# Kernel tuning notes

Hardware: AMD Instinct MI355X
Metric: run time of the kernel (lower is better)

The kernel has to match this reference:

```python
import jax, jax.numpy as jnp
import numpy as np

HEADS = 16

def setup_inputs() -> dict:
    key = jax.random.key(0)
    ks = jax.random.split(key, 8)
    S, B, D = 2048, 2, 1024
    scale = 0.02
    return {
        'query': jax.random.normal(ks[0], (S, B, D), jnp.float32),
        'key':   jax.random.normal(ks[1], (S, B, D), jnp.float32),
        'value': jax.random.normal(ks[2], (S, B, D), jnp.float32),
        'Wq': jax.random.normal(ks[3], (D, D), jnp.float32) * scale,
        'bq': jnp.zeros((D,), jnp.float32),
        'Wk': jax.random.normal(ks[4], (D, D), jnp.float32) * scale,
        'bk': jnp.zeros((D,), jnp.float32),
        'Wv': jax.random.normal(ks[5], (D, D), jnp.float32) * scale,
        'bv': jnp.zeros((D,), jnp.float32),
        'Wo': jax.random.normal(ks[6], (D, D), jnp.float32) * scale,
        'bo': jnp.zeros((D,), jnp.float32),
    }

def reference(query, key, value, Wq, bq, Wk, bk, Wv, bv, Wo, bo):
    S, B, D = query.shape
    h = HEADS
    dk = D // h
    # projections: nn.Linear stores weight [out, in] -> x @ W.T + b
    q = (query @ Wq.T + bq).reshape(S, B, h, dk)
    k = (key   @ Wk.T + bk).reshape(S, B, h, dk)
    v = (value @ Wv.T + bv).reshape(S, B, h, dk)
    # scores: [i, j, b, h]
    scores = jnp.einsum('ibhd,jbhd->ijbh', q, k) / jnp.sqrt(jnp.asarray(dk, q.dtype))
    # original uses nn.Softmax(dim=1) -> softmax over key axis j
    attn = jax.nn.softmax(scores, axis=1)
    x = jnp.einsum('ijbh,jbhd->ibhd', attn, v).reshape(S, B, D)
    return x @ Wo.T + bo
```

## Files before the change

### kernel.cpp

```cpp
#include <hip/hip_runtime.h>
#include <hip/hip_bf16.h>
#include <math.h>

#define S_LEN  2048
#define NBATCH 2
#define DMODEL 1024
#define NHEADS 16
#define HDIM   64
#define MROWS  (S_LEN*NBATCH)
#define NBH    (NBATCH*NHEADS)

typedef __attribute__((ext_vector_type(8))) short          bf16x8;
typedef __attribute__((ext_vector_type(4))) float          f32x4;
typedef __attribute__((ext_vector_type(8))) unsigned short u16x8;

__device__ __forceinline__ unsigned short f2bf(float x) {
    union { __hip_bfloat16 h; unsigned short u; } c;
    c.h = __float2bfloat16(x);
    return c.u;
}
__device__ __forceinline__ unsigned int pk2(float a, float b) {
    return (unsigned int)f2bf(a) | ((unsigned int)f2bf(b) << 16);
}

__global__ __launch_bounds__(256)
void cvt7(const float* __restrict__ s0, const float* __restrict__ s1,
          const float* __restrict__ s2, const float* __restrict__ s3,
          const float* __restrict__ s4, const float* __restrict__ s5,
          const float* __restrict__ s6,
          unsigned short* __restrict__ d0, unsigned short* __restrict__ d1,
          unsigned short* __restrict__ d2, unsigned short* __restrict__ d3,
          unsigned short* __restrict__ d4, unsigned short* __restrict__ d5,
          unsigned short* __restrict__ d6)
{
    const float* s; unsigned short* d; int n;
    switch (blockIdx.y) {
        case 0: s = s0; d = d0; n = MROWS*DMODEL;  break;
        case 1: s = s1; d = d1; n = MROWS*DMODEL;  break;
        case 2: s = s2; d = d2; n = MROWS*DMODEL;  break;
        case 3: s = s3; d = d3; n = DMODEL*DMODEL; break;
        case 4: s = s4; d = d4; n = DMODEL*DMODEL; break;
        case 5: s = s5; d = d5; n = DMODEL*DMODEL; break;
        default: s = s6; d = d6; n = DMODEL*DMODEL; break;
    }
    int i = (blockIdx.x*256 + threadIdx.x) * 8;
    if (i >= n) return;
    float4 a = *(const float4*)(s + i);
    float4 b = *(const float4*)(s + i + 4);
    u16x8 o;
    o[0] = f2bf(a.x); o[1] = f2bf(a.y); o[2] = f2bf(a.z); o[3] = f2bf(a.w);
    o[4] = f2bf(b.x); o[5] = f2bf(b.y); o[6] = f2bf(b.z); o[7] = f2bf(b.w);
    *(u16x8*)(d + i) = o;
}

#define GBM 128
#define GBN 128
#define GBK 32

__device__ __forceinline__ void gemm_bf16_core(
    const unsigned short* __restrict__ A,
    const unsigned short* __restrict__ W,
    const float* __restrict__ bias,
    float* __restrict__ Cf, unsigned short* __restrict__ Cb,
    int mode, float scale)
{
    __shared__ __align__(16) unsigned short As[GBM*GBK];
    __shared__ __align__(16) unsigned short Bs[GBN*GBK];

    const int tid = threadIdx.x;
    const int l   = tid & 63;
    const int w   = tid >> 6;
    const int m0  = blockIdx.y * GBM;
    const int n0  = blockIdx.x * GBN;
    const int wm  = (w >> 1) * 64;
    const int wn  = (w & 1) * 64;

    f32x4 acc[4][4];
    #pragma unroll
    for (int i = 0; i < 4; ++i)
        #pragma unroll
        for (int j = 0; j < 4; ++j)
            acc[i][j] = (f32x4){0.f, 0.f, 0.f, 0.f};

    const int srow = l >> 2;
    const int scol = (l & 3) * 8;

    for (int k0 = 0; k0 < DMODEL; k0 += GBK) {
        #pragma unroll
        for (int i = 0; i < 2; ++i) {
            int c = w*2 + i;
            const unsigned short* ga = A + (size_t)(m0 + c*16 + srow)*DMODEL + k0 + scol;
            const unsigned short* gb = W + (size_t)(n0 + c*16 + srow)*DMODEL + k0 + scol;
            __builtin_amdgcn_global_load_lds(
                (const __attribute__((address_space(1))) void*)ga,
                (__attribute__((address_space(3))) void*)(As + c*512), 16, 0, 0);
            __builtin_amdgcn_global_load_lds(
                (const __attribute__((address_space(1))) void*)gb,
                (__attribute__((address_space(3))) void*)(Bs + c*512), 16, 0, 0);
        }
        __syncthreads();

        bf16x8 af[4], bfr[4];
        #pragma unroll
        for (int f = 0; f < 4; ++f) {
            af[f]  = *(const bf16x8*)(As + (wm + f*16 + (l & 15))*GBK + (l >> 4)*8);
            bfr[f] = *(const bf16x8*)(Bs + (wn + f*16 + (l & 15))*GBK + (l >> 4)*8);
        }
        #pragma unroll
        for (int i = 0; i < 4; ++i)
            #pragma unroll
            for (int j = 0; j < 4; ++j)
                acc[i][j] = __builtin_amdgcn_mfma_f32_16x16x32_bf16(af[i], bfr[j], acc[i][j], 0, 0, 0);
        __syncthreads();
    }

    const int col_l = l & 15;
    const int row_l = (l >> 4) * 4;
    #pragma unroll
    for (int j = 0; j < 4; ++j) {
        int col = n0 + wn + j*16 + col_l;
        float bv = bias[col];
        #pragma unroll
        for (int i = 0; i < 4; ++i) {
            int mbase = m0 + wm + i*16 + row_l;
            #pragma unroll
            for (int r = 0; r < 4; ++r) {
                int m = mbase + r;
                float vout = (acc[i][j][r] + bv) * scale;
                if (mode == 0) {
                    Cf[(size_t)m*DMODEL + col] = vout;
                } else {
                    int s = m >> 1, b = m & 1;
                    int h = col >> 6, d = col & 63;
                    if (mode == 1)
                        Cb[((size_t)(b*NHEADS + h)*S_LEN + s)*HDIM + d] = f2bf(vout);
                    else
                        Cb[((size_t)(b*NHEADS + h)*HDIM + d)*S_LEN + s] = f2bf(vout);
                }
            }
        }
    }
}

__global__ __launch_bounds__(256)
void gemm_qkv_bf16(const unsigned short* __restrict__ qb, const unsigned short* __restrict__ kb,
                   const unsigned short* __restrict__ vb,
                   const unsigned short* __restrict__ Wqb, const float* __restrict__ bq,
                   const unsigned short* __restrict__ Wkb, const float* __restrict__ bk,
                   const unsigned short* __restrict__ Wvb, const float* __restrict__ bv,
                   unsigned short* __restrict__ qp, unsigned short* __restrict__ kp,
                   unsigned short* __restrict__ vt)
{
    const int z = blockIdx.z;
    const unsigned short* A = (z==0) ? qb  : (z==1) ? kb  : vb;
    const unsigned short* W = (z==0) ? Wqb : (z==1) ? Wkb : Wvb;
    const float* bias       = (z==0) ? bq  : (z==1) ? bk  : bv;
    unsigned short* C       = (z==0) ? qp  : (z==1) ? kp  : vt;
    int   mode  = (z==2) ? 2 : 1;
    float scale = (z==0) ? 0.125f : 1.0f;
    gemm_bf16_core(A, W, bias, nullptr, C, mode, scale);
}

__global__ __launch_bounds__(256)
void gemm_out_bf16(const unsigned short* __restrict__ A, const unsigned short* __restrict__ W,
                   const float* __restrict__ bias, float* __restrict__ C)
{
    gemm_bf16_core(A, W, bias, C, nullptr, 0, 1.0f);
}

#define QBLK  128
#define KVBLK 64

__global__ __launch_bounds__(256)
void attn_mfma(const unsigned short* __restrict__ qp, const unsigned short* __restrict__ kp,
               const unsigned short* __restrict__ vt, unsigned short* __restrict__ x)
{
    __shared__ __align__(16) unsigned short Ks[KVBLK*HDIM];
    __shared__ __align__(16) unsigned short Vs[HDIM*KVBLK];
    __shared__ __align__(16) unsigned short Ps[4][32*KVBLK];

    const int tid = threadIdx.x;
    const int w   = tid >> 6;
    const int l   = tid & 63;
    const int g   = l >> 4;
    const int s16 = l & 15;
    const int q0  = blockIdx.x * QBLK;
    const int bh  = blockIdx.y;
    const int b   = bh >> 4;
    const int h   = bh & 15;
    const size_t base = (size_t)bh * S_LEN * HDIM;

    char* KsB = (char*)Ks;
    char* VsB = (char*)Vs;
    char* PsB = (char*)&Ps[w][0];

    bf16x8 qf[2][2];
    #pragma unroll
    for (int ni = 0; ni < 2; ++ni)
        #pragma unroll
        for (int ks = 0; ks < 2; ++ks) {
            int qrow = q0 + w*32 + ni*16 + s16;
            qf[ni][ks] = *(const bf16x8*)(qp + base + (size_t)qrow*HDIM + ks*32 + g*8);
        }

    f32x4 oacc[2][4];
    #pragma unroll
    for (int ni = 0; ni < 2; ++ni)
        #pragma unroll
        for (int nj = 0; nj < 4; ++nj)
            oacc[ni][nj] = (f32x4){0.f, 0.f, 0.f, 0.f};
    float run_m[2] = {-1e30f, -1e30f};
    float run_l[2] = {0.f, 0.f};

    for (int kt = 0; kt < S_LEN; kt += KVBLK) {
        #pragma unroll
        for (int it = 0; it < 2; ++it) {
            int idx  = it*256 + tid;
            int row  = idx >> 3;
            int u    = (idx & 7) ^ (row & 7);
            const unsigned short* gk = kp + base + (size_t)(kt + row)*HDIM + u*8;
            __builtin_amdgcn_global_load_lds(
                (const __attribute__((address_space(1))) void*)gk,
                (__attribute__((address_space(3))) void*)(Ks + (it*256 + w*64)*8), 16, 0, 0);
            const unsigned short* gv = vt + base + (size_t)row*S_LEN + kt + u*8;
            __builtin_amdgcn_global_load_lds(
                (const __attribute__((address_space(1))) void*)gv,
                (__attribute__((address_space(3))) void*)(Vs + (it*256 + w*64)*8), 16, 0, 0);
        }
        __syncthreads();

        f32x4 sacc[4][2];
        #pragma unroll
        for (int mi = 0; mi < 4; ++mi)
            #pragma unroll
            for (int ni = 0; ni < 2; ++ni)
                sacc[mi][ni] = (f32x4){0.f, 0.f, 0.f, 0.f};

        #pragma unroll
        for (int ks = 0; ks < 2; ++ks) {
            bf16x8 af[4];
            #pragma unroll
            for (int mi = 0; mi < 4; ++mi) {
                int key  = mi*16 + s16;
                int addr = ((key << 7) + (ks << 6) + (g << 4)) ^ ((key & 7) << 4);
                af[mi] = *(const bf16x8*)(KsB + addr);
            }
            #pragma unroll
            for (int mi = 0; mi < 4; ++mi)
                #pragma unroll
                for (int ni = 0; ni < 2; ++ni)
                    sacc[mi][ni] = __builtin_amdgcn_mfma_f32_16x16x32_bf16(
                        af[mi], qf[ni][ks], sacc[mi][ni], 0, 0, 0);
        }

        float al[2];
        #pragma unroll
        for (int ni = 0; ni < 2; ++ni) {
            float tm = -1e30f;
            #pragma unroll
            for (int mi = 0; mi < 4; ++mi)
                #pragma unroll
                for (int r = 0; r < 4; ++r)
                    tm = fmaxf(tm, sacc[mi][ni][r]);
            tm = fmaxf(tm, __shfl_xor(tm, 16));
            tm = fmaxf(tm, __shfl_xor(tm, 32));
            float mn = fmaxf(run_m[ni], tm);
            al[ni] = __expf(run_m[ni] - mn);
            float ps = 0.f;
            int row = ni*16 + s16;
            #pragma unroll
            for (int mi = 0; mi < 4; ++mi) {
                float p0 = __expf(sacc[mi][ni][0] - mn);
                float p1 = __expf(sacc[mi][ni][1] - mn);
                float p2 = __expf(sacc[mi][ni][2] - mn);
                float p3 = __expf(sacc[mi][ni][3] - mn);
                ps += (p0 + p1) + (p2 + p3);
                uint2 wv; wv.x = pk2(p0, p1); wv.y = pk2(p2, p3);
                int addr = ((row << 7) + (mi << 5) + (g << 3)) ^ ((row & 7) << 4);
                *(uint2*)(PsB + addr) = wv;
            }
            ps += __shfl_xor(ps, 16);
            ps += __shfl_xor(ps, 32);
            run_l[ni] = run_l[ni]*al[ni] + ps;
            run_m[ni] = mn;
        }

        float alo[2][4];
        #pragma unroll
        for (int ni = 0; ni < 2; ++ni)
            #pragma unroll
            for (int r = 0; r < 4; ++r)
                alo[ni][r] = __shfl(al[ni], 20*g + r);
        #pragma unroll
        for (int ni = 0; ni < 2; ++ni)
            #pragma unroll
            for (int nj = 0; nj < 4; ++nj)
                #pragma unroll
                for (int r = 0; r < 4; ++r)
                    oacc[ni][nj][r] *= alo[ni][r];

        #pragma unroll
        for (int ks = 0; ks < 2; ++ks) {
            bf16x8 pa[2];
            #pragma unroll
            for (int ni = 0; ni < 2; ++ni) {
                int row  = ni*16 + s16;
                int addr = ((row << 7) + (ks << 6) + (g << 4)) ^ ((row & 7) << 4);
                pa[ni] = *(const bf16x8*)(PsB + addr);
            }
            bf16x8 bv[4];
            #pragma unroll
            for (int nj = 0; nj < 4; ++nj) {
                int d    = nj*16 + s16;
                int addr = ((d << 7) + (ks << 6) + (g << 4)) ^ ((d & 7) << 4);
                bv[nj] = *(const bf16x8*)(VsB + addr);
            }
            #pragma unroll
            for (int ni = 0; ni < 2; ++ni)
                #pragma unroll
                for (int nj = 0; nj < 4; ++nj)
                    oacc[ni][nj] = __builtin_amdgcn_mfma_f32_16x16x32_bf16(
                        pa[ni], bv[nj], oacc[ni][nj], 0, 0, 0);
        }
        __syncthreads();
    }

    #pragma unroll
    for (int ni = 0; ni < 2; ++ni) {
        #pragma unroll
        for (int r = 0; r < 4; ++r) {
            float rl  = __shfl(run_l[ni], 20*g + r);
            float inv = 1.f / rl;
            int row = q0 + w*32 + ni*16 + 4*g + r;
            #pragma unroll
            for (int nj = 0; nj < 4; ++nj) {
                int col = h*HDIM + nj*16 + s16;
                x[(size_t)(row*NBATCH + b)*DMODEL + col] = f2bf(oacc[ni][nj][r] * inv);
            }
        }
    }
}

extern "C" void kernel_launch(void* const* d_in, const int* in_sizes, int n_in,
                              void* d_out, int out_size, void* d_ws, size_t ws_size,
                              hipStream_t stream)
{
    const float* query = (const float*)d_in[0];
    const float* key_i = (const float*)d_in[1];
    const float* value = (const float*)d_in[2];
    const float* Wq = (const float*)d_in[3];
    const float* bq = (const float*)d_in[4];
    const float* Wk = (const float*)d_in[5];
    const float* bk = (const float*)d_in[6];
    const float* Wv = (const float*)d_in[7];
    const float* bv = (const float*)d_in[8];
    const float* Wo = (const float*)d_in[9];
    const float* bo = (const float*)d_in[10];
    float* out = (float*)d_out;

    char* ws = (char*)d_ws;
    unsigned short* qb  = (unsigned short*)(ws);
    unsigned short* kb2 = (unsigned short*)(ws + (size_t) 8*1024*1024);
    unsigned short* vb  = (unsigned short*)(ws + (size_t)16*1024*1024);
    unsigned short* Wqb = (unsigned short*)(ws + (size_t)24*1024*1024);
    unsigned short* Wkb = (unsigned short*)(ws + (size_t)26*1024*1024);
    unsigned short* Wvb = (unsigned short*)(ws + (size_t)28*1024*1024);
    unsigned short* Wob = (unsigned short*)(ws + (size_t)30*1024*1024);
    unsigned short* qp  = (unsigned short*)(ws + (size_t)32*1024*1024);
    unsigned short* kp  = (unsigned short*)(ws + (size_t)40*1024*1024);
    unsigned short* vt  = (unsigned short*)(ws + (size_t)48*1024*1024);
    unsigned short* xab = (unsigned short*)(ws + (size_t)56*1024*1024);

    dim3 gCvt(MROWS*DMODEL/(256*8), 7);
    cvt7<<<gCvt, 256, 0, stream>>>(query, key_i, value, Wq, Wk, Wv, Wo,
                                   qb, kb2, vb, Wqb, Wkb, Wvb, Wob);

    dim3 gProj(DMODEL/GBN, MROWS/GBM, 3);
    gemm_qkv_bf16<<<gProj, 256, 0, stream>>>(qb, kb2, vb,
                                             Wqb, bq, Wkb, bk, Wvb, bv,
                                             qp, kp, vt);

    dim3 gAttn(S_LEN/QBLK, NBH);
    attn_mfma<<<gAttn, 256, 0, stream>>>(qp, kp, vt, xab);

    dim3 gOut(DMODEL/GBN, MROWS/GBM, 1);
    gemm_out_bf16<<<gOut, 256, 0, stream>>>(xab, Wob, bo, out);
}
```

Before: 259.6 us.

## Double-buffer K/V tiles in attention and coalesce transposed V stores via LDS

The attention loop now double-buffers its K and V shared-memory tiles, so the async global-to-LDS load for the next tile is issued while the current tile is computed, and one barrier per iteration is dropped. The V projection is split into its own kernel that stages the output tile in shared memory and writes the transposed layout as 16-byte vector stores instead of scattered 2-byte stores. GEMM modes become template parameters. This doubles K/V LDS use in attention, which may lower occupancy, and adds one kernel launch.

New measurement: 270.1 us. 4.0% more time.

```diff
diff --git a/kernel.cpp b/kernel.cpp
--- a/kernel.cpp
+++ b/kernel.cpp
@@ -57,12 +57,13 @@
 #define GBN 128
 #define GBK 32
 
+template<int MODE>
 __device__ __forceinline__ void gemm_bf16_core(
     const unsigned short* __restrict__ A,
     const unsigned short* __restrict__ W,
     const float* __restrict__ bias,
     float* __restrict__ Cf, unsigned short* __restrict__ Cb,
-    int mode, float scale)
+    float scale)
 {
     __shared__ __align__(16) unsigned short As[GBM*GBK];
     __shared__ __align__(16) unsigned short Bs[GBN*GBK];
@@ -116,6 +117,44 @@
 
     const int col_l = l & 15;
     const int row_l = (l >> 4) * 4;
+
+    if constexpr (MODE == 2) {
+        __shared__ __align__(16) unsigned short tileS[64][136];
+        #pragma unroll
+        for (int ph = 0; ph < 2; ++ph) {
+            __syncthreads();
+            if ((w >> 1) == ph) {
+                #pragma unroll
+                for (int j = 0; j < 4; ++j) {
+                    int c = wn + j*16 + col_l;
+                    float bv = bias[n0 + c];
+                    #pragma unroll
+                    for (int i = 0; i < 4; ++i)
+                        #pragma unroll
+                        for (int r = 0; r < 4; ++r)
+                            tileS[i*16 + row_l + r][c] = f2bf((acc[i][j][r] + bv) * scale);
+                }
+            }
+            __syncthreads();
+            const int sbase = (m0 + ph*64) >> 1;
+            #pragma unroll
+            for (int it = 0; it < 4; ++it) {
+                int idx = it*256 + tid;
+                int c    = idx >> 3;
+                int bb   = (idx >> 2) & 1;
+                int sl0  = (idx & 3) * 8;
+                int hh   = (n0 + c) >> 6;
+                int dd   = (n0 + c) & 63;
+                u16x8 ov;
+                #pragma unroll
+                for (int k2 = 0; k2 < 8; ++k2)
+                    ov[k2] = tileS[2*(sl0 + k2) + bb][c];
+                *(u16x8*)(Cb + ((size_t)(bb*NHEADS + hh)*HDIM + dd)*S_LEN + sbase + sl0) = ov;
+            }
+        }
+        return;
+    }
+
     #pragma unroll
     for (int j = 0; j < 4; ++j) {
         int col = n0 + wn + j*16 + col_l;
@@ -127,15 +166,12 @@
             for (int r = 0; r < 4; ++r) {
                 int m = mbase + r;
                 float vout = (acc[i][j][r] + bv) * scale;
-                if (mode == 0) {
+                if constexpr (MODE == 0) {
                     Cf[(size_t)m*DMODEL + col] = vout;
                 } else {
                     int s = m >> 1, b = m & 1;
                     int h = col >> 6, d = col & 63;
-                    if (mode == 1)
-                        Cb[((size_t)(b*NHEADS + h)*S_LEN + s)*HDIM + d] = f2bf(vout);
-                    else
-                        Cb[((size_t)(b*NHEADS + h)*HDIM + d)*S_LEN + s] = f2bf(vout);
+                    Cb[((size_t)(b*NHEADS + h)*S_LEN + s)*HDIM + d] = f2bf(vout);
                 }
             }
         }
@@ -143,40 +179,44 @@
 }
 
 __global__ __launch_bounds__(256)
-void gemm_qkv_bf16(const unsigned short* __restrict__ qb, const unsigned short* __restrict__ kb,
-                   const unsigned short* __restrict__ vb,
-                   const unsigned short* __restrict__ Wqb, const float* __restrict__ bq,
-                   const unsigned short* __restrict__ Wkb, const float* __restrict__ bk,
-                   const unsigned short* __restrict__ Wvb, const float* __restrict__ bv,
-                   unsigned short* __restrict__ qp, unsigned short* __restrict__ kp,
-                   unsigned short* __restrict__ vt)
+void gemm_qk(const unsigned short* __restrict__ qb, const unsigned short* __restrict__ kb,
+             const unsigned short* __restrict__ Wqb, const float* __restrict__ bq,
+             const unsigned short* __restrict__ Wkb, const float* __restrict__ bk,
+             unsigned short* __restrict__ qp, unsigned short* __restrict__ kp)
 {
     const int z = blockIdx.z;
-    const unsigned short* A = (z==0) ? qb  : (z==1) ? kb  : vb;
-    const unsigned short* W = (z==0) ? Wqb : (z==1) ? Wkb : Wvb;
-    const float* bias       = (z==0) ? bq  : (z==1) ? bk  : bv;
-    unsigned short* C       = (z==0) ? qp  : (z==1) ? kp  : vt;
-    int   mode  = (z==2) ? 2 : 1;
-    float scale = (z==0) ? 0.125f : 1.0f;
-    gemm_bf16_core(A, W, bias, nullptr, C, mode, scale);
+    const unsigned short* A = (z==0) ? qb  : kb;
+    const unsigned short* W = (z==0) ? Wqb : Wkb;
+    const float* bias       = (z==0) ? bq  : bk;
+    unsigned short* C       = (z==0) ? qp  : kp;
+    float scale             = (z==0) ? 0.125f : 1.0f;
+    gemm_bf16_core<1>(A, W, bias, nullptr, C, scale);
+}
+
+__global__ __launch_bounds__(256)
+void gemm_vt(const unsigned short* __restrict__ vb, const unsigned short* __restrict__ Wvb,
+             const float* __restrict__ bv, unsigned short* __restrict__ vt)
+{
+    gemm_bf16_core<2>(vb, Wvb, bv, nullptr, vt, 1.0f);
 }
 
 __global__ __launch_bounds__(256)
 void gemm_out_bf16(const unsigned short* __restrict__ A, const unsigned short* __restrict__ W,
                    const float* __restrict__ bias, float* __restrict__ C)
 {
-    gemm_bf16_core(A, W, bias, C, nullptr, 0, 1.0f);
+    gemm_bf16_core<0>(A, W, bias, C, nullptr, 1.0f);
 }
 
 #define QBLK  128
 #define KVBLK 64
+#define NT    (S_LEN/KVBLK)
 
 __global__ __launch_bounds__(256)
 void attn_mfma(const unsigned short* __restrict__ qp, const unsigned short* __restrict__ kp,
                const unsigned short* __restrict__ vt, unsigned short* __restrict__ x)
 {
-    __shared__ __align__(16) unsigned short Ks[KVBLK*HDIM];
-    __shared__ __align__(16) unsigned short Vs[HDIM*KVBLK];
+    __shared__ __align__(16) unsigned short Ks[2][KVBLK*HDIM];
+    __shared__ __align__(16) unsigned short Vs[2][KVBLK*HDIM];
     __shared__ __align__(16) unsigned short Ps[4][32*KVBLK];
 
     const int tid = threadIdx.x;
@@ -190,9 +230,26 @@
     const int h   = bh & 15;
     const size_t base = (size_t)bh * S_LEN * HDIM;
 
-    char* KsB = (char*)Ks;
-    char* VsB = (char*)Vs;
     char* PsB = (char*)&Ps[w][0];
+
+#define STAGE(buf, kt_) do {                                                        \
+    _Pragma("unroll")                                                               \
+    for (int it_ = 0; it_ < 2; ++it_) {                                             \
+        int idx_ = it_*256 + tid;                                                   \
+        int row_ = idx_ >> 3;                                                       \
+        int u_   = (idx_ & 7) ^ (row_ & 7);                                         \
+        const unsigned short* gk_ = kp + base + (size_t)((kt_) + row_)*HDIM + u_*8; \
+        __builtin_amdgcn_global_load_lds(                                           \
+            (const __attribute__((address_space(1))) void*)gk_,                     \
+            (__attribute__((address_space(3))) void*)(Ks[buf] + (it_*256 + w*64)*8),\
+            16, 0, 0);                                                              \
+        const unsigned short* gv_ = vt + base + (size_t)row_*S_LEN + (kt_) + u_*8;  \
+        __builtin_amdgcn_global_load_lds(                                           \
+            (const __attribute__((address_space(1))) void*)gv_,                     \
+            (__attribute__((address_space(3))) void*)(Vs[buf] + (it_*256 + w*64)*8),\
+            16, 0, 0);                                                              \
+    }                                                                               \
+} while (0)
 
     bf16x8 qf[2][2];
     #pragma unroll
@@ -212,22 +269,15 @@
     float run_m[2] = {-1e30f, -1e30f};
     float run_l[2] = {0.f, 0.f};
 
-    for (int kt = 0; kt < S_LEN; kt += KVBLK) {
-        #pragma unroll
-        for (int it = 0; it < 2; ++it) {
-            int idx  = it*256 + tid;
-            int row  = idx >> 3;
-            int u    = (idx & 7) ^ (row & 7);
-            const unsigned short* gk = kp + base + (size_t)(kt + row)*HDIM + u*8;
-            __builtin_amdgcn_global_load_lds(
-                (const __attribute__((address_space(1))) void*)gk,
-                (__attribute__((address_space(3))) void*)(Ks + (it*256 + w*64)*8), 16, 0, 0);
-            const unsigned short* gv = vt + base + (size_t)row*S_LEN + kt + u*8;
-            __builtin_amdgcn_global_load_lds(
-                (const __attribute__((address_space(1))) void*)gv,
-                (__attribute__((address_space(3))) void*)(Vs + (it*256 + w*64)*8), 16, 0, 0);
-        }
+    STAGE(0, 0);
+
+    for (int t = 0; t < NT; ++t) {
+        const int cur = t & 1;
         __syncthreads();
+        if (t + 1 < NT) STAGE(cur ^ 1, (t + 1)*KVBLK);
+
+        const char* KsB = (const char*)Ks[cur];
+        const char* VsB = (const char*)Vs[cur];
 
         f32x4 sacc[4][2];
         #pragma unroll
@@ -322,8 +372,8 @@
                     oacc[ni][nj] = __builtin_amdgcn_mfma_f32_16x16x32_bf16(
                         pa[ni], bv[nj], oacc[ni][nj], 0, 0, 0);
         }
-        __syncthreads();
-    }
+    }
+#undef STAGE
 
     #pragma unroll
     for (int ni = 0; ni < 2; ++ni) {
@@ -375,10 +425,11 @@
     cvt7<<<gCvt, 256, 0, stream>>>(query, key_i, value, Wq, Wk, Wv, Wo,
                                    qb, kb2, vb, Wqb, Wkb, Wvb, Wob);
 
-    dim3 gProj(DMODEL/GBN, MROWS/GBM, 3);
-    gemm_qkv_bf16<<<gProj, 256, 0, stream>>>(qb, kb2, vb,
-                                             Wqb, bq, Wkb, bk, Wvb, bv,
-                                             qp, kp, vt);
+    dim3 gQK(DMODEL/GBN, MROWS/GBM, 2);
+    gemm_qk<<<gQK, 256, 0, stream>>>(qb, kb2, Wqb, bq, Wkb, bk, qp, kp);
+
+    dim3 gV(DMODEL/GBN, MROWS/GBM);
+    gemm_vt<<<gV, 256, 0, stream>>>(vb, Wvb, bv, vt);
 
     dim3 gAttn(S_LEN/QBLK, NBH);
     attn_mfma<<<gAttn, 256, 0, stream>>>(qp, kp, vt, xab);
```
